# Kernel optimization log

Measured on AMD Instinct MI355X. Metric: run time of the kernel, lower is better.

Reference implementation:

```python
import jax, jax.numpy as jnp
import numpy as np

B, C, H, W = 8, 256, 64, 64
NUM_HEADS = 4


def setup_inputs() -> dict:
    key = jax.random.key(0)
    ks = jax.random.split(key, 6)
    s = 0.02  # small init scale for 1x1 conv weights
    return {
        "x": jax.random.normal(ks[0], (B, C, H, W), jnp.float32),
        "cproj": jax.random.normal(ks[1], (B, C, H, W), jnp.float32),
        "wq": jax.random.normal(ks[2], (C, C), jnp.float32) * s,
        "bq": jnp.zeros((C,), jnp.float32),
        "wkv": jax.random.normal(ks[3], (2 * C, C), jnp.float32) * s,
        "bkv": jnp.zeros((2 * C,), jnp.float32),
        "wo": jax.random.normal(ks[4], (C, C), jnp.float32) * s,  # zero_module in torch; random here for a meaningful baseline
        "bo": jnp.zeros((C,), jnp.float32),
    }


def reference(x, cproj, wq, bq, wkv, bkv, wo, bo):
    Bb, Cc, Hh, Ww = x.shape
    N = Hh * Ww
    h = NUM_HEADS
    d = Cc // h
    scale = 1.0 / jnp.sqrt(jnp.sqrt(jnp.asarray(Cc, jnp.float32)))

    xf = x.reshape(Bb, Cc, N)
    cf = cproj.reshape(Bb, Cc, N)

    # 1x1 convs == channel matmuls
    Q = jnp.einsum('oc,bcn->bon', wq, xf) + bq[None, :, None]           # (B,C,N)
    KV = jnp.einsum('oc,bcn->bon', wkv, cf) + bkv[None, :, None]        # (B,2C,N)
    K, V = KV[:, :Cc], KV[:, Cc:]

    # softmax over channel-dim-within-head for q, over spatial N for k
    q = jax.nn.softmax(Q.reshape(Bb, h, d, N) * scale, axis=2).reshape(Bb, Cc, N)
    k = jax.nn.softmax(K.reshape(Bb, h, d, N), axis=3).reshape(Bb, Cc, N)

    # linear-attention: (B,C,C) context, then project back to N — note heads are mixed, per original bmm
    context = jnp.einsum('bcn,bdn->bcd', k, V)
    out = jnp.einsum('bcd,bdn->bcn', context, q)

    out = jnp.einsum('oc,bcn->bon', wo, out) + bo[None, :, None]
    return out.reshape(Bb, Cc, Hh, Ww)
```

## Files before the change

### kernel.cpp

```cpp
#include <hip/hip_runtime.h>

#define B_ 8
#define C_ 256
#define N_ 4096
#define H_ 4
#define KVC_ 512
#define NSPLIT 8

typedef float f32x4 __attribute__((ext_vector_type(4)));
typedef __bf16 bf16x8 __attribute__((ext_vector_type(8)));
typedef unsigned short u16x8 __attribute__((ext_vector_type(8)));
typedef unsigned short u16x4 __attribute__((ext_vector_type(4)));

union BU8 { u16x8 u; bf16x8 b; };

__device__ __forceinline__ unsigned short f2bf(float f) {
  unsigned u = __float_as_uint(f);
  u += 0x7fff + ((u >> 16) & 1);
  return (unsigned short)(u >> 16);
}

__device__ __forceinline__ f32x4 mfma16(bf16x8 a, bf16x8 b, f32x4 c) {
  return __builtin_amdgcn_mfma_f32_16x16x32_bf16(a, b, c, 0, 0, 0);
}

__global__ __launch_bounds__(256) void qproj_softmax(
    const float* __restrict__ wq, const float* __restrict__ x,
    const float* __restrict__ bq, unsigned short* __restrict__ qT) {
  __shared__ unsigned short As[256][40];
  __shared__ unsigned short Bs[32][68];
  __shared__ float bql[C_];
  const int b = blockIdx.z;
  const int n0 = blockIdx.x * 64;
  const int tid = threadIdx.x;
  const int lane = tid & 63, w = tid >> 6;
  const float* xb = x + (size_t)b * C_ * N_;

  bql[tid] = bq[tid];

  f32x4 acc[16];
#pragma unroll
  for (int i = 0; i < 16; i++) acc[i] = (f32x4){0.f, 0.f, 0.f, 0.f};

  const int colL = lane & 15, kq = lane >> 4;
  for (int kc = 0; kc < C_; kc += 32) {
    __syncthreads();
#pragma unroll
    for (int i = 0; i < 8; i++) {
      int r = i * 32 + (tid >> 3), c = (tid & 7) * 4;
      float4 v = *(const float4*)&wq[r * C_ + kc + c];
      *(u16x4*)&As[r][c] = (u16x4){f2bf(v.x), f2bf(v.y), f2bf(v.z), f2bf(v.w)};
    }
#pragma unroll
    for (int i = 0; i < 2; i++) {
      int r = i * 16 + (tid >> 4), c = (tid & 15) * 4;
      float4 v = *(const float4*)&xb[(size_t)(kc + r) * N_ + n0 + c];
      *(u16x4*)&Bs[r][c] = (u16x4){f2bf(v.x), f2bf(v.y), f2bf(v.z), f2bf(v.w)};
    }
    __syncthreads();

    BU8 bu;
#pragma unroll
    for (int j = 0; j < 8; j++) bu.u[j] = Bs[kq * 8 + j][w * 16 + colL];
    bf16x8 bf = bu.b;
#pragma unroll
    for (int mt = 0; mt < 16; mt++) {
      bf16x8 af = *(const bf16x8*)&As[mt * 16 + colL][kq * 8];
      acc[mt] = mfma16(af, bf, acc[mt]);
    }
  }

  const int quad = lane >> 4;
  const int n = n0 + w * 16 + colL;
  unsigned short* qbase = qT + ((size_t)b * N_ + n) * C_;
#pragma unroll
  for (int h = 0; h < H_; h++) {
    float v[16];
    float mx = -1e30f;
#pragma unroll
    for (int i = 0; i < 4; i++) {
      int mt = 4 * h + i;
#pragma unroll
      for (int r = 0; r < 4; r++) {
        int m = mt * 16 + quad * 4 + r;
        float val = (acc[mt][r] + bql[m]) * 0.25f;
        v[i * 4 + r] = val;
        mx = fmaxf(mx, val);
      }
    }
    mx = fmaxf(mx, __shfl_xor(mx, 16));
    mx = fmaxf(mx, __shfl_xor(mx, 32));
    float s = 0.f;
#pragma unroll
    for (int j = 0; j < 16; j++) { v[j] = __expf(v[j] - mx); s += v[j]; }
    s += __shfl_xor(s, 16);
    s += __shfl_xor(s, 32);
    float inv = 1.0f / s;
#pragma unroll
    for (int i = 0; i < 4; i++) {
      u16x4 o = (u16x4){f2bf(v[i * 4 + 0] * inv), f2bf(v[i * 4 + 1] * inv),
                        f2bf(v[i * 4 + 2] * inv), f2bf(v[i * 4 + 3] * inv)};
      *(u16x4*)(qbase + (4 * h + i) * 16 + quad * 4) = o;
    }
  }
}

__global__ __launch_bounds__(256) void kvproj(
    const float* __restrict__ wkv, const float* __restrict__ cp,
    const float* __restrict__ bkv, float* __restrict__ Kf,
    unsigned short* __restrict__ Vb) {
  __shared__ unsigned short As[128][40];
  __shared__ unsigned short Bs[32][136];
  const int b = blockIdx.z;
  const int m0 = blockIdx.y * 128, n0 = blockIdx.x * 128;
  const int tid = threadIdx.x, lane = tid & 63, w = tid >> 6;
  const int m0w = (w >> 1) * 64, n0w = (w & 1) * 64;
  const int colL = lane & 15, kq = lane >> 4;
  const float* cpb = cp + (size_t)b * C_ * N_;

  f32x4 acc[4][4];
#pragma unroll
  for (int i = 0; i < 4; i++)
#pragma unroll
    for (int j = 0; j < 4; j++) acc[i][j] = (f32x4){0.f, 0.f, 0.f, 0.f};

  for (int kc = 0; kc < C_; kc += 32) {
    __syncthreads();
#pragma unroll
    for (int i = 0; i < 4; i++) {
      int r = i * 32 + (tid >> 3), c = (tid & 7) * 4;
      float4 v = *(const float4*)&wkv[(size_t)(m0 + r) * C_ + kc + c];
      *(u16x4*)&As[r][c] = (u16x4){f2bf(v.x), f2bf(v.y), f2bf(v.z), f2bf(v.w)};
    }
#pragma unroll
    for (int i = 0; i < 4; i++) {
      int r = i * 8 + (tid >> 5), c = (tid & 31) * 4;
      float4 v = *(const float4*)&cpb[(size_t)(kc + r) * N_ + n0 + c];
      *(u16x4*)&Bs[r][c] = (u16x4){f2bf(v.x), f2bf(v.y), f2bf(v.z), f2bf(v.w)};
    }
    __syncthreads();

    bf16x8 bfr[4];
#pragma unroll
    for (int nt = 0; nt < 4; nt++) {
      BU8 bu;
#pragma unroll
      for (int j = 0; j < 8; j++) bu.u[j] = Bs[kq * 8 + j][n0w + nt * 16 + colL];
      bfr[nt] = bu.b;
    }
#pragma unroll
    for (int mt = 0; mt < 4; mt++) {
      bf16x8 af = *(const bf16x8*)&As[m0w + mt * 16 + colL][kq * 8];
#pragma unroll
      for (int nt = 0; nt < 4; nt++) acc[mt][nt] = mfma16(af, bfr[nt], acc[mt][nt]);
    }
  }

  const int quad = lane >> 4;
#pragma unroll
  for (int mt = 0; mt < 4; mt++) {
#pragma unroll
    for (int r = 0; r < 4; r++) {
      int m = m0 + m0w + mt * 16 + quad * 4 + r;
      float bias = bkv[m];
#pragma unroll
      for (int nt = 0; nt < 4; nt++) {
        int n = n0 + n0w + nt * 16 + colL;
        float val = acc[mt][nt][r] + bias;
        if (m0 < C_) {
          Kf[((size_t)b * C_ + m) * N_ + n] = val;
        } else {
          Vb[((size_t)b * C_ + (m - C_)) * N_ + n] = f2bf(val);
        }
      }
    }
  }
}

__global__ __launch_bounds__(256) void ksoftmax(const float* __restrict__ Kf,
                                                unsigned short* __restrict__ kb) {
  const int b = blockIdx.x >> 8, c = blockIdx.x & 255;
  const float* row = Kf + ((size_t)b * C_ + c) * N_;
  unsigned short* orow = kb + ((size_t)b * C_ + c) * N_;
  const int t = threadIdx.x, lane = t & 63, wv = t >> 6;
  __shared__ float red[8];

  float4 v[4];
  float mx = -1e30f;
#pragma unroll
  for (int i = 0; i < 4; i++) {
    v[i] = *(const float4*)&row[i * 1024 + t * 4];
    mx = fmaxf(fmaxf(fmaxf(mx, v[i].x), fmaxf(v[i].y, v[i].z)), v[i].w);
  }
#pragma unroll
  for (int o = 32; o > 0; o >>= 1) mx = fmaxf(mx, __shfl_down(mx, o));
  if (lane == 0) red[wv] = mx;
  __syncthreads();
  mx = fmaxf(fmaxf(red[0], red[1]), fmaxf(red[2], red[3]));

  float s = 0.f;
#pragma unroll
  for (int i = 0; i < 4; i++) {
    v[i].x = __expf(v[i].x - mx); v[i].y = __expf(v[i].y - mx);
    v[i].z = __expf(v[i].z - mx); v[i].w = __expf(v[i].w - mx);
    s += v[i].x + v[i].y + v[i].z + v[i].w;
  }
#pragma unroll
  for (int o = 32; o > 0; o >>= 1) s += __shfl_down(s, o);
  if (lane == 0) red[4 + wv] = s;
  __syncthreads();
  float inv = 1.0f / (red[4] + red[5] + red[6] + red[7]);
#pragma unroll
  for (int i = 0; i < 4; i++) {
    u16x4 o = (u16x4){f2bf(v[i].x * inv), f2bf(v[i].y * inv),
                      f2bf(v[i].z * inv), f2bf(v[i].w * inv)};
    *(u16x4*)&orow[i * 1024 + t * 4] = o;
  }
}

__global__ __launch_bounds__(256) void ctx_part(
    const unsigned short* __restrict__ kb, const unsigned short* __restrict__ Vb,
    float* __restrict__ ctxp) {
  __shared__ unsigned short As[128][40];
  __shared__ unsigned short Bs[128][40];
  const int z = blockIdx.z, b = z >> 3, s = z & 7;
  const int m0 = blockIdx.y * 128, n0 = blockIdx.x * 128;
  const int tid = threadIdx.x, lane = tid & 63, w = tid >> 6;
  const int m0w = (w >> 1) * 64, n0w = (w & 1) * 64;
  const int colL = lane & 15, kq = lane >> 4;
  const unsigned short* Ab = kb + (size_t)b * C_ * N_;
  const unsigned short* Bb = Vb + (size_t)b * C_ * N_;

  f32x4 acc[4][4];
#pragma unroll
  for (int i = 0; i < 4; i++)
#pragma unroll
    for (int j = 0; j < 4; j++) acc[i][j] = (f32x4){0.f, 0.f, 0.f, 0.f};

  const int kbeg = s * (N_ / NSPLIT);
  for (int kc = kbeg; kc < kbeg + N_ / NSPLIT; kc += 32) {
    __syncthreads();
#pragma unroll
    for (int i = 0; i < 2; i++) {
      int r = i * 64 + (tid >> 2), c = (tid & 3) * 8;
      *(u16x8*)&As[r][c] = *(const u16x8*)&Ab[(size_t)(m0 + r) * N_ + kc + c];
      *(u16x8*)&Bs[r][c] = *(const u16x8*)&Bb[(size_t)(n0 + r) * N_ + kc + c];
    }
    __syncthreads();

    bf16x8 af[4], bfr[4];
#pragma unroll
    for (int mt = 0; mt < 4; mt++) af[mt] = *(const bf16x8*)&As[m0w + mt * 16 + colL][kq * 8];
#pragma unroll
    for (int nt = 0; nt < 4; nt++) bfr[nt] = *(const bf16x8*)&Bs[n0w + nt * 16 + colL][kq * 8];
#pragma unroll
    for (int mt = 0; mt < 4; mt++)
#pragma unroll
      for (int nt = 0; nt < 4; nt++) acc[mt][nt] = mfma16(af[mt], bfr[nt], acc[mt][nt]);
  }

  float* outp = ctxp + ((size_t)s * B_ + b) * C_ * C_;
  const int quad = lane >> 4;
#pragma unroll
  for (int mt = 0; mt < 4; mt++)
#pragma unroll
    for (int nt = 0; nt < 4; nt++)
#pragma unroll
      for (int r = 0; r < 4; r++) {
        int m = m0 + m0w + mt * 16 + quad * 4 + r;
        int n = n0 + n0w + nt * 16 + colL;
        outp[(size_t)m * C_ + n] = acc[mt][nt][r];
      }
}

__global__ __launch_bounds__(256) void ctx_reduce(const float* __restrict__ ctxp,
                                                  unsigned short* __restrict__ ctxs) {
  const size_t e = ((size_t)blockIdx.x * 256 + threadIdx.x) * 4;
  float4 a = {0.f, 0.f, 0.f, 0.f};
#pragma unroll
  for (int s = 0; s < NSPLIT; s++) {
    float4 v = *(const float4*)&ctxp[(size_t)s * B_ * C_ * C_ + e];
    a.x += v.x; a.y += v.y; a.z += v.z; a.w += v.w;
  }
  *(u16x4*)&ctxs[e] = (u16x4){f2bf(a.x), f2bf(a.y), f2bf(a.z), f2bf(a.w)};
}

__global__ __launch_bounds__(256) void oproj(const float* __restrict__ wo,
                                             const unsigned short* __restrict__ ctxs,
                                             unsigned short* __restrict__ ctx2) {
  __shared__ unsigned short As[128][40];
  __shared__ unsigned short Bs[32][136];
  const int b = blockIdx.z;
  const int m0 = blockIdx.y * 128, n0 = blockIdx.x * 128;
  const int tid = threadIdx.x, lane = tid & 63, w = tid >> 6;
  const int m0w = (w >> 1) * 64, n0w = (w & 1) * 64;
  const int colL = lane & 15, kq = lane >> 4;
  const unsigned short* cb = ctxs + (size_t)b * C_ * C_;

  f32x4 acc[4][4];
#pragma unroll
  for (int i = 0; i < 4; i++)
#pragma unroll
    for (int j = 0; j < 4; j++) acc[i][j] = (f32x4){0.f, 0.f, 0.f, 0.f};

  for (int kc = 0; kc < C_; kc += 32) {
    __syncthreads();
#pragma unroll
    for (int i = 0; i < 4; i++) {
      int r = i * 32 + (tid >> 3), c = (tid & 7) * 4;
      float4 v = *(const float4*)&wo[(size_t)(m0 + r) * C_ + kc + c];
      *(u16x4*)&As[r][c] = (u16x4){f2bf(v.x), f2bf(v.y), f2bf(v.z), f2bf(v.w)};
    }
#pragma unroll
    for (int i = 0; i < 2; i++) {
      int r = i * 16 + (tid >> 4), c = (tid & 15) * 8;
      *(u16x8*)&Bs[r][c] = *(const u16x8*)&cb[(size_t)(kc + r) * C_ + n0 + c];
    }
    __syncthreads();

    bf16x8 bfr[4];
#pragma unroll
    for (int nt = 0; nt < 4; nt++) {
      BU8 bu;
#pragma unroll
      for (int j = 0; j < 8; j++) bu.u[j] = Bs[kq * 8 + j][n0w + nt * 16 + colL];
      bfr[nt] = bu.b;
    }
#pragma unroll
    for (int mt = 0; mt < 4; mt++) {
      bf16x8 af = *(const bf16x8*)&As[m0w + mt * 16 + colL][kq * 8];
#pragma unroll
      for (int nt = 0; nt < 4; nt++) acc[mt][nt] = mfma16(af, bfr[nt], acc[mt][nt]);
    }
  }

  unsigned short* ob = ctx2 + (size_t)b * C_ * C_;
  const int quad = lane >> 4;
#pragma unroll
  for (int mt = 0; mt < 4; mt++)
#pragma unroll
    for (int nt = 0; nt < 4; nt++)
#pragma unroll
      for (int r = 0; r < 4; r++) {
        int m = m0 + m0w + mt * 16 + quad * 4 + r;
        int n = n0 + n0w + nt * 16 + colL;
        ob[(size_t)m * C_ + n] = f2bf(acc[mt][nt][r]);
      }
}

__global__ __launch_bounds__(256) void outgemm(const unsigned short* __restrict__ ctx2,
                                               const unsigned short* __restrict__ qT,
                                               const float* __restrict__ bo,
                                               float* __restrict__ out) {
  __shared__ unsigned short As[128][40];
  __shared__ unsigned short Bs[128][40];
  const int b = blockIdx.z;
  const int n0 = blockIdx.x * 128, m0 = blockIdx.y * 128;
  const int tid = threadIdx.x, lane = tid & 63, w = tid >> 6;
  const int m0w = (w >> 1) * 64, n0w = (w & 1) * 64;
  const int colL = lane & 15, kq = lane >> 4;
  const unsigned short* Ab = ctx2 + (size_t)b * C_ * C_;
  const unsigned short* Bb = qT + (size_t)b * N_ * C_;

  f32x4 acc[4][4];
#pragma unroll
  for (int i = 0; i < 4; i++)
#pragma unroll
    for (int j = 0; j < 4; j++) acc[i][j] = (f32x4){0.f, 0.f, 0.f, 0.f};

  for (int kc = 0; kc < C_; kc += 32) {
    __syncthreads();
#pragma unroll
    for (int i = 0; i < 2; i++) {
      int r = i * 64 + (tid >> 2), c = (tid & 3) * 8;
      *(u16x8*)&As[r][c] = *(const u16x8*)&Ab[(size_t)(m0 + r) * C_ + kc + c];
      *(u16x8*)&Bs[r][c] = *(const u16x8*)&Bb[(size_t)(n0 + r) * C_ + kc + c];
    }
    __syncthreads();

    bf16x8 af[4], bfr[4];
#pragma unroll
    for (int mt = 0; mt < 4; mt++) af[mt] = *(const bf16x8*)&As[m0w + mt * 16 + colL][kq * 8];
#pragma unroll
    for (int nt = 0; nt < 4; nt++) bfr[nt] = *(const bf16x8*)&Bs[n0w + nt * 16 + colL][kq * 8];
#pragma unroll
    for (int mt = 0; mt < 4; mt++)
#pragma unroll
      for (int nt = 0; nt < 4; nt++) acc[mt][nt] = mfma16(af[mt], bfr[nt], acc[mt][nt]);
  }

  float* ob = out + (size_t)b * C_ * N_;
  const int quad = lane >> 4;
#pragma unroll
  for (int mt = 0; mt < 4; mt++)
#pragma unroll
    for (int r = 0; r < 4; r++) {
      int m = m0 + m0w + mt * 16 + quad * 4 + r;
      float bias = bo[m];
#pragma unroll
      for (int nt = 0; nt < 4; nt++) {
        int n = n0 + n0w + nt * 16 + colL;
        ob[(size_t)m * N_ + n] = acc[mt][nt][r] + bias;
      }
    }
}

extern "C" void kernel_launch(void* const* d_in, const int* in_sizes, int n_in,
                              void* d_out, int out_size, void* d_ws, size_t ws_size,
                              hipStream_t stream) {
  const float* x     = (const float*)d_in[0];
  const float* cproj = (const float*)d_in[1];
  const float* wq    = (const float*)d_in[2];
  const float* bq    = (const float*)d_in[3];
  const float* wkv   = (const float*)d_in[4];
  const float* bkv   = (const float*)d_in[5];
  const float* wo    = (const float*)d_in[6];
  const float* bo    = (const float*)d_in[7];
  float* out = (float*)d_out;

  unsigned short* qT   = (unsigned short*)d_ws;
  float*          Kf   = (float*)(qT + (size_t)B_ * N_ * C_);
  unsigned short* Vb   = (unsigned short*)(Kf + (size_t)B_ * C_ * N_);
  unsigned short* kb   = Vb + (size_t)B_ * C_ * N_;
  float*          ctxp = (float*)(kb + (size_t)B_ * C_ * N_);
  unsigned short* ctxs = (unsigned short*)(ctxp + (size_t)NSPLIT * B_ * C_ * C_);
  unsigned short* ctx2 = ctxs + (size_t)B_ * C_ * C_;

  qproj_softmax<<<dim3(N_ / 64, 1, B_), 256, 0, stream>>>(wq, x, bq, qT);
  kvproj<<<dim3(N_ / 128, KVC_ / 128, B_), 256, 0, stream>>>(wkv, cproj, bkv, Kf, Vb);
  ksoftmax<<<dim3(B_ * C_), 256, 0, stream>>>(Kf, kb);
  ctx_part<<<dim3(2, 2, B_ * NSPLIT), 256, 0, stream>>>(kb, Vb, ctxp);
  ctx_reduce<<<dim3(B_ * C_ * C_ / 1024), 256, 0, stream>>>(ctxp, ctxs);
  oproj<<<dim3(2, 2, B_), 256, 0, stream>>>(wo, ctxs, ctx2);
  outgemm<<<dim3(N_ / 128, 2, B_), 256, 0, stream>>>(ctx2, qT, bo, out);
}
```

Measured before the change: 216.8 us.

## Pre-cast inputs to bf16 K-major and stage GEMM tiles with direct-to-LDS loads

Adds kernels that cast the weights to bf16 and transpose-cast x and cproj into N-major bf16 layouts. All GEMMs then stage 64-wide K tiles into XOR-swizzled LDS through global_load_lds, which removes the per-element LDS gathers and the in-loop float-to-bf16 conversion. The q projection is retiled to 128x128 blocks, ctx_part uses narrower tiles for more blocks, and the context reduce now writes a transposed result. Workspace buffers are aliased to save memory. The cost is two extra launches and an extra pass over the inputs for the transpose.

```diff
diff --git a/kernel.cpp b/kernel.cpp
--- a/kernel.cpp
+++ b/kernel.cpp
@@ -3,8 +3,6 @@
 #define B_ 8
 #define C_ 256
 #define N_ 4096
-#define H_ 4
-#define KVC_ 512
 #define NSPLIT 8
 
 typedef float f32x4 __attribute__((ext_vector_type(4)));
@@ -12,8 +10,6 @@
 typedef unsigned short u16x8 __attribute__((ext_vector_type(8)));
 typedef unsigned short u16x4 __attribute__((ext_vector_type(4)));
 
-union BU8 { u16x8 u; bf16x8 b; };
-
 __device__ __forceinline__ unsigned short f2bf(float f) {
   unsigned u = __float_as_uint(f);
   u += 0x7fff + ((u >> 16) & 1);
@@ -24,70 +20,118 @@
   return __builtin_amdgcn_mfma_f32_16x16x32_bf16(a, b, c, 0, 0, 0);
 }
 
-__global__ __launch_bounds__(256) void qproj_softmax(
-    const float* __restrict__ wq, const float* __restrict__ x,
+typedef __attribute__((address_space(1))) const void* gvp;
+typedef __attribute__((address_space(3))) void* lvp;
+__device__ __forceinline__ void gld16(const void* g, void* l) {
+  __builtin_amdgcn_global_load_lds((gvp)g, (lvp)l, 16, 0, 0);
+}
+
+template <int ROWS>
+__device__ __forceinline__ void stage(unsigned short* lds, const unsigned short* g,
+                                      int ld, int w, int lane) {
+  const int r8 = lane >> 3;
+  const int ce = ((lane & 7) ^ r8) << 3;
+  const unsigned short* gp = g + (size_t)(w * (ROWS / 4) + r8) * ld + ce;
+  unsigned short* lp = lds + w * (ROWS / 4) * 64;
+#pragma unroll
+  for (int i = 0; i < ROWS / 32; i++)
+    gld16(gp + (size_t)(i * 8) * ld, lp + i * 512);
+}
+
+__device__ __forceinline__ bf16x8 frag(const unsigned short* lds, int row, int kc) {
+  return *(const bf16x8*)(lds + row * 64 + ((kc ^ (row & 7)) << 3));
+}
+
+__global__ __launch_bounds__(256) void castw(
+    const float* __restrict__ wq, const float* __restrict__ wkv,
+    const float* __restrict__ wo, unsigned short* __restrict__ wqb,
+    unsigned short* __restrict__ wkvb, unsigned short* __restrict__ wob) {
+  int i = (blockIdx.x * 256 + threadIdx.x) * 4;
+  const float* src;
+  unsigned short* dst;
+  int off;
+  if (i < 65536) { src = wq; dst = wqb; off = i; }
+  else if (i < 196608) { src = wkv; dst = wkvb; off = i - 65536; }
+  else { src = wo; dst = wob; off = i - 196608; }
+  float4 v = *(const float4*)(src + off);
+  *(u16x4*)(dst + off) = (u16x4){f2bf(v.x), f2bf(v.y), f2bf(v.z), f2bf(v.w)};
+}
+
+__global__ __launch_bounds__(256) void transpose_cast(
+    const float* __restrict__ x, const float* __restrict__ cp,
+    unsigned short* __restrict__ xT, unsigned short* __restrict__ cpT) {
+  __shared__ unsigned short tr[64][72];
+  const int z = blockIdx.z, b = z >> 1;
+  const float* src = (z & 1) ? cp : x;
+  unsigned short* dst = (z & 1) ? cpT : xT;
+  const int c0 = blockIdx.y * 64, n0 = blockIdx.x * 64;
+  const int t = threadIdx.x;
+  const int row = t >> 2, cg = (t & 3) * 16;
+  const float* sp = src + ((size_t)b * C_ + c0 + row) * N_ + n0 + cg;
+#pragma unroll
+  for (int j = 0; j < 16; j += 4) {
+    float4 v = *(const float4*)(sp + j);
+    tr[cg + j + 0][row] = f2bf(v.x);
+    tr[cg + j + 1][row] = f2bf(v.y);
+    tr[cg + j + 2][row] = f2bf(v.z);
+    tr[cg + j + 3][row] = f2bf(v.w);
+  }
+  __syncthreads();
+  unsigned short* dp = dst + ((size_t)b * N_ + n0 + row) * C_ + c0 + cg;
+  *(u16x8*)dp = *(const u16x8*)&tr[row][cg];
+  *(u16x8*)(dp + 8) = *(const u16x8*)&tr[row][cg + 8];
+}
+
+__global__ __launch_bounds__(256) void qproj(
+    const unsigned short* __restrict__ wqb, const unsigned short* __restrict__ xT,
     const float* __restrict__ bq, unsigned short* __restrict__ qT) {
-  __shared__ unsigned short As[256][40];
-  __shared__ unsigned short Bs[32][68];
-  __shared__ float bql[C_];
-  const int b = blockIdx.z;
-  const int n0 = blockIdx.x * 64;
-  const int tid = threadIdx.x;
-  const int lane = tid & 63, w = tid >> 6;
-  const float* xb = x + (size_t)b * C_ * N_;
-
-  bql[tid] = bq[tid];
-
-  f32x4 acc[16];
-#pragma unroll
-  for (int i = 0; i < 16; i++) acc[i] = (f32x4){0.f, 0.f, 0.f, 0.f};
-
-  const int colL = lane & 15, kq = lane >> 4;
-  for (int kc = 0; kc < C_; kc += 32) {
-    __syncthreads();
-#pragma unroll
-    for (int i = 0; i < 8; i++) {
-      int r = i * 32 + (tid >> 3), c = (tid & 7) * 4;
-      float4 v = *(const float4*)&wq[r * C_ + kc + c];
-      *(u16x4*)&As[r][c] = (u16x4){f2bf(v.x), f2bf(v.y), f2bf(v.z), f2bf(v.w)};
-    }
-#pragma unroll
-    for (int i = 0; i < 2; i++) {
-      int r = i * 16 + (tid >> 4), c = (tid & 15) * 4;
-      float4 v = *(const float4*)&xb[(size_t)(kc + r) * N_ + n0 + c];
-      *(u16x4*)&Bs[r][c] = (u16x4){f2bf(v.x), f2bf(v.y), f2bf(v.z), f2bf(v.w)};
-    }
-    __syncthreads();
-
-    BU8 bu;
-#pragma unroll
-    for (int j = 0; j < 8; j++) bu.u[j] = Bs[kq * 8 + j][w * 16 + colL];
-    bf16x8 bf = bu.b;
-#pragma unroll
-    for (int mt = 0; mt < 16; mt++) {
-      bf16x8 af = *(const bf16x8*)&As[mt * 16 + colL][kq * 8];
-      acc[mt] = mfma16(af, bf, acc[mt]);
-    }
-  }
-
-  const int quad = lane >> 4;
-  const int n = n0 + w * 16 + colL;
-  unsigned short* qbase = qT + ((size_t)b * N_ + n) * C_;
-#pragma unroll
-  for (int h = 0; h < H_; h++) {
+  __shared__ __align__(16) unsigned short As[128 * 64];
+  __shared__ __align__(16) unsigned short Bs[128 * 64];
+  const int b = blockIdx.z, m0 = blockIdx.y * 128, n0 = blockIdx.x * 128;
+  const int tid = threadIdx.x, lane = tid & 63, w = tid >> 6;
+  const int m0w = (w >> 1) * 64, n0w = (w & 1) * 64;
+  const int colL = lane & 15, kq = lane >> 4, quad = lane >> 4;
+  const unsigned short* Ag = wqb + (size_t)m0 * C_;
+  const unsigned short* Bg = xT + ((size_t)b * N_ + n0) * C_;
+
+  f32x4 acc[4][4];
+#pragma unroll
+  for (int i = 0; i < 4; i++)
+#pragma unroll
+    for (int j = 0; j < 4; j++) acc[i][j] = (f32x4){0.f, 0.f, 0.f, 0.f};
+
+  for (int kt = 0; kt < 4; kt++) {
+    stage<128>(As, Ag + kt * 64, C_, w, lane);
+    stage<128>(Bs, Bg + kt * 64, C_, w, lane);
+    __syncthreads();
+#pragma unroll
+    for (int ks = 0; ks < 2; ks++) {
+      bf16x8 af[4], bf[4];
+#pragma unroll
+      for (int mt = 0; mt < 4; mt++) af[mt] = frag(As, m0w + mt * 16 + colL, ks * 4 + kq);
+#pragma unroll
+      for (int nt = 0; nt < 4; nt++) bf[nt] = frag(Bs, n0w + nt * 16 + colL, ks * 4 + kq);
+#pragma unroll
+      for (int mt = 0; mt < 4; mt++)
+#pragma unroll
+        for (int nt = 0; nt < 4; nt++) acc[mt][nt] = mfma16(af[mt], bf[nt], acc[mt][nt]);
+    }
+    __syncthreads();
+  }
+
+#pragma unroll
+  for (int nt = 0; nt < 4; nt++) {
     float v[16];
     float mx = -1e30f;
 #pragma unroll
-    for (int i = 0; i < 4; i++) {
-      int mt = 4 * h + i;
+    for (int mt = 0; mt < 4; mt++)
 #pragma unroll
       for (int r = 0; r < 4; r++) {
-        int m = mt * 16 + quad * 4 + r;
-        float val = (acc[mt][r] + bql[m]) * 0.25f;
-        v[i * 4 + r] = val;
+        int m = m0 + m0w + mt * 16 + quad * 4 + r;
+        float val = (acc[mt][nt][r] + bq[m]) * 0.25f;
+        v[mt * 4 + r] = val;
         mx = fmaxf(mx, val);
       }
-    }
     mx = fmaxf(mx, __shfl_xor(mx, 16));
     mx = fmaxf(mx, __shfl_xor(mx, 32));
     float s = 0.f;
@@ -96,27 +140,29 @@
     s += __shfl_xor(s, 16);
     s += __shfl_xor(s, 32);
     float inv = 1.0f / s;
-#pragma unroll
-    for (int i = 0; i < 4; i++) {
-      u16x4 o = (u16x4){f2bf(v[i * 4 + 0] * inv), f2bf(v[i * 4 + 1] * inv),
-                        f2bf(v[i * 4 + 2] * inv), f2bf(v[i * 4 + 3] * inv)};
-      *(u16x4*)(qbase + (4 * h + i) * 16 + quad * 4) = o;
+    const int n = n0 + n0w + nt * 16 + colL;
+    unsigned short* qb = qT + ((size_t)b * N_ + n) * C_ + m0 + m0w;
+#pragma unroll
+    for (int mt = 0; mt < 4; mt++) {
+      u16x4 o = (u16x4){f2bf(v[mt * 4 + 0] * inv), f2bf(v[mt * 4 + 1] * inv),
+                        f2bf(v[mt * 4 + 2] * inv), f2bf(v[mt * 4 + 3] * inv)};
+      *(u16x4*)(qb + mt * 16 + quad * 4) = o;
     }
   }
 }
 
 __global__ __launch_bounds__(256) void kvproj(
-    const float* __restrict__ wkv, const float* __restrict__ cp,
+    const unsigned short* __restrict__ wkvb, const unsigned short* __restrict__ cpT,
     const float* __restrict__ bkv, float* __restrict__ Kf,
     unsigned short* __restrict__ Vb) {
-  __shared__ unsigned short As[128][40];
-  __shared__ unsigned short Bs[32][136];
-  const int b = blockIdx.z;
-  const int m0 = blockIdx.y * 128, n0 = blockIdx.x * 128;
+  __shared__ __align__(16) unsigned short As[128 * 64];
+  __shared__ __align__(16) unsigned short Bs[128 * 64];
+  const int b = blockIdx.z, m0 = blockIdx.y * 128, n0 = blockIdx.x * 128;
   const int tid = threadIdx.x, lane = tid & 63, w = tid >> 6;
   const int m0w = (w >> 1) * 64, n0w = (w & 1) * 64;
-  const int colL = lane & 15, kq = lane >> 4;
-  const float* cpb = cp + (size_t)b * C_ * N_;
+  const int colL = lane & 15, kq = lane >> 4, quad = lane >> 4;
+  const unsigned short* Ag = wkvb + (size_t)m0 * C_;
+  const unsigned short* Bg = cpT + ((size_t)b * N_ + n0) * C_;
 
   f32x4 acc[4][4];
 #pragma unroll
@@ -124,57 +170,41 @@
 #pragma unroll
     for (int j = 0; j < 4; j++) acc[i][j] = (f32x4){0.f, 0.f, 0.f, 0.f};
 
-  for (int kc = 0; kc < C_; kc += 32) {
-    __syncthreads();
-#pragma unroll
-    for (int i = 0; i < 4; i++) {
-      int r = i * 32 + (tid >> 3), c = (tid & 7) * 4;
-      float4 v = *(const float4*)&wkv[(size_t)(m0 + r) * C_ + kc + c];
-      *(u16x4*)&As[r][c] = (u16x4){f2bf(v.x), f2bf(v.y), f2bf(v.z), f2bf(v.w)};
-    }
-#pragma unroll
-    for (int i = 0; i < 4; i++) {
-      int r = i * 8 + (tid >> 5), c = (tid & 31) * 4;
-      float4 v = *(const float4*)&cpb[(size_t)(kc + r) * N_ + n0 + c];
-      *(u16x4*)&Bs[r][c] = (u16x4){f2bf(v.x), f2bf(v.y), f2bf(v.z), f2bf(v.w)};
-    }
-    __syncthreads();
-
-    bf16x8 bfr[4];
-#pragma unroll
-    for (int nt = 0; nt < 4; nt++) {
-      BU8 bu;
-#pragma unroll
-      for (int j = 0; j < 8; j++) bu.u[j] = Bs[kq * 8 + j][n0w + nt * 16 + colL];
-      bfr[nt] = bu.b;
-    }
-#pragma unroll
-    for (int mt = 0; mt < 4; mt++) {
-      bf16x8 af = *(const bf16x8*)&As[m0w + mt * 16 + colL][kq * 8];
-#pragma unroll
-      for (int nt = 0; nt < 4; nt++) acc[mt][nt] = mfma16(af, bfr[nt], acc[mt][nt]);
-    }
-  }
-
-  const int quad = lane >> 4;
-#pragma unroll
-  for (int mt = 0; mt < 4; mt++) {
+  for (int kt = 0; kt < 4; kt++) {
+    stage<128>(As, Ag + kt * 64, C_, w, lane);
+    stage<128>(Bs, Bg + kt * 64, C_, w, lane);
+    __syncthreads();
+#pragma unroll
+    for (int ks = 0; ks < 2; ks++) {
+      bf16x8 af[4], bf[4];
+#pragma unroll
+      for (int mt = 0; mt < 4; mt++) af[mt] = frag(As, m0w + mt * 16 + colL, ks * 4 + kq);
+#pragma unroll
+      for (int nt = 0; nt < 4; nt++) bf[nt] = frag(Bs, n0w + nt * 16 + colL, ks * 4 + kq);
+#pragma unroll
+      for (int mt = 0; mt < 4; mt++)
+#pragma unroll
+        for (int nt = 0; nt < 4; nt++) acc[mt][nt] = mfma16(af[mt], bf[nt], acc[mt][nt]);
+    }
+    __syncthreads();
+  }
+
+#pragma unroll
+  for (int mt = 0; mt < 4; mt++)
 #pragma unroll
     for (int r = 0; r < 4; r++) {
       int m = m0 + m0w + mt * 16 + quad * 4 + r;
       float bias = bkv[m];
-#pragma unroll
-      for (int nt = 0; nt < 4; nt++) {
-        int n = n0 + n0w + nt * 16 + colL;
-        float val = acc[mt][nt][r] + bias;
-        if (m0 < C_) {
-          Kf[((size_t)b * C_ + m) * N_ + n] = val;
-        } else {
-          Vb[((size_t)b * C_ + (m - C_)) * N_ + n] = f2bf(val);
-        }
+      if (m < C_) {
+        float* kr = Kf + ((size_t)b * C_ + m) * N_ + n0 + n0w;
+#pragma unroll
+        for (int nt = 0; nt < 4; nt++) kr[nt * 16 + colL] = acc[mt][nt][r] + bias;
+      } else {
+        unsigned short* vr = Vb + ((size_t)b * C_ + m - C_) * N_ + n0 + n0w;
+#pragma unroll
+        for (int nt = 0; nt < 4; nt++) vr[nt * 16 + colL] = f2bf(acc[mt][nt][r] + bias);
       }
     }
-  }
 }
 
 __global__ __launch_bounds__(256) void ksoftmax(const float* __restrict__ Kf,
@@ -221,50 +251,47 @@
 __global__ __launch_bounds__(256) void ctx_part(
     const unsigned short* __restrict__ kb, const unsigned short* __restrict__ Vb,
     float* __restrict__ ctxp) {
-  __shared__ unsigned short As[128][40];
-  __shared__ unsigned short Bs[128][40];
+  __shared__ __align__(16) unsigned short As[128 * 64];
+  __shared__ __align__(16) unsigned short Bs[64 * 64];
   const int z = blockIdx.z, b = z >> 3, s = z & 7;
-  const int m0 = blockIdx.y * 128, n0 = blockIdx.x * 128;
+  const int m0 = blockIdx.y * 128, n0 = blockIdx.x * 64;
   const int tid = threadIdx.x, lane = tid & 63, w = tid >> 6;
-  const int m0w = (w >> 1) * 64, n0w = (w & 1) * 64;
-  const int colL = lane & 15, kq = lane >> 4;
-  const unsigned short* Ab = kb + (size_t)b * C_ * N_;
-  const unsigned short* Bb = Vb + (size_t)b * C_ * N_;
-
-  f32x4 acc[4][4];
+  const int m0w = (w & 1) * 64, n0w = (w >> 1) * 32;
+  const int colL = lane & 15, kq = lane >> 4, quad = lane >> 4;
+  const unsigned short* Ag = kb + ((size_t)b * C_ + m0) * N_;
+  const unsigned short* Bg = Vb + ((size_t)b * C_ + n0) * N_;
+  const int kbeg = s * (N_ / NSPLIT);
+
+  f32x4 acc[4][2];
 #pragma unroll
   for (int i = 0; i < 4; i++)
 #pragma unroll
-    for (int j = 0; j < 4; j++) acc[i][j] = (f32x4){0.f, 0.f, 0.f, 0.f};
-
-  const int kbeg = s * (N_ / NSPLIT);
-  for (int kc = kbeg; kc < kbeg + N_ / NSPLIT; kc += 32) {
-    __syncthreads();
-#pragma unroll
-    for (int i = 0; i < 2; i++) {
-      int r = i * 64 + (tid >> 2), c = (tid & 3) * 8;
-      *(u16x8*)&As[r][c] = *(const u16x8*)&Ab[(size_t)(m0 + r) * N_ + kc + c];
-      *(u16x8*)&Bs[r][c] = *(const u16x8*)&Bb[(size_t)(n0 + r) * N_ + kc + c];
-    }
-    __syncthreads();
-
-    bf16x8 af[4], bfr[4];
-#pragma unroll
-    for (int mt = 0; mt < 4; mt++) af[mt] = *(const bf16x8*)&As[m0w + mt * 16 + colL][kq * 8];
-#pragma unroll
-    for (int nt = 0; nt < 4; nt++) bfr[nt] = *(const bf16x8*)&Bs[n0w + nt * 16 + colL][kq * 8];
-#pragma unroll
-    for (int mt = 0; mt < 4; mt++)
-#pragma unroll
-      for (int nt = 0; nt < 4; nt++) acc[mt][nt] = mfma16(af[mt], bfr[nt], acc[mt][nt]);
+    for (int j = 0; j < 2; j++) acc[i][j] = (f32x4){0.f, 0.f, 0.f, 0.f};
+
+  for (int kt = 0; kt < (N_ / NSPLIT) / 64; kt++) {
+    stage<128>(As, Ag + kbeg + kt * 64, N_, w, lane);
+    stage<64>(Bs, Bg + kbeg + kt * 64, N_, w, lane);
+    __syncthreads();
+#pragma unroll
+    for (int ks = 0; ks < 2; ks++) {
+      bf16x8 af[4], bf[2];
+#pragma unroll
+      for (int mt = 0; mt < 4; mt++) af[mt] = frag(As, m0w + mt * 16 + colL, ks * 4 + kq);
+#pragma unroll
+      for (int nt = 0; nt < 2; nt++) bf[nt] = frag(Bs, n0w + nt * 16 + colL, ks * 4 + kq);
+#pragma unroll
+      for (int mt = 0; mt < 4; mt++)
+#pragma unroll
+        for (int nt = 0; nt < 2; nt++) acc[mt][nt] = mfma16(af[mt], bf[nt], acc[mt][nt]);
+    }
+    __syncthreads();
   }
 
   float* outp = ctxp + ((size_t)s * B_ + b) * C_ * C_;
-  const int quad = lane >> 4;
 #pragma unroll
   for (int mt = 0; mt < 4; mt++)
 #pragma unroll
-    for (int nt = 0; nt < 4; nt++)
+    for (int nt = 0; nt < 2; nt++)
 #pragma unroll
       for (int r = 0; r < 4; r++) {
         int m = m0 + m0w + mt * 16 + quad * 4 + r;
@@ -273,29 +300,44 @@
       }
 }
 
-__global__ __launch_bounds__(256) void ctx_reduce(const float* __restrict__ ctxp,
-                                                  unsigned short* __restrict__ ctxs) {
-  const size_t e = ((size_t)blockIdx.x * 256 + threadIdx.x) * 4;
-  float4 a = {0.f, 0.f, 0.f, 0.f};
-#pragma unroll
+__global__ __launch_bounds__(256) void ctx_reduce_t(const float* __restrict__ ctxp,
+                                                    unsigned short* __restrict__ ctxsT) {
+  __shared__ unsigned short t[64][72];
+  const int b = blockIdx.z, c0 = blockIdx.y * 64, d0 = blockIdx.x * 64;
+  const int tid = threadIdx.x;
+  const int cl = tid >> 2, dg = (tid & 3) * 16;
+  const float* base = ctxp + ((size_t)b * C_ + c0 + cl) * C_ + d0 + dg;
+  float acc[16];
+#pragma unroll
+  for (int j = 0; j < 16; j++) acc[j] = 0.f;
   for (int s = 0; s < NSPLIT; s++) {
-    float4 v = *(const float4*)&ctxp[(size_t)s * B_ * C_ * C_ + e];
-    a.x += v.x; a.y += v.y; a.z += v.z; a.w += v.w;
-  }
-  *(u16x4*)&ctxs[e] = (u16x4){f2bf(a.x), f2bf(a.y), f2bf(a.z), f2bf(a.w)};
-}
-
-__global__ __launch_bounds__(256) void oproj(const float* __restrict__ wo,
-                                             const unsigned short* __restrict__ ctxs,
-                                             unsigned short* __restrict__ ctx2) {
-  __shared__ unsigned short As[128][40];
-  __shared__ unsigned short Bs[32][136];
-  const int b = blockIdx.z;
-  const int m0 = blockIdx.y * 128, n0 = blockIdx.x * 128;
+    const float* p = base + (size_t)s * B_ * C_ * C_;
+#pragma unroll
+    for (int j = 0; j < 16; j += 4) {
+      float4 v = *(const float4*)(p + j);
+      acc[j] += v.x; acc[j + 1] += v.y; acc[j + 2] += v.z; acc[j + 3] += v.w;
+    }
+  }
+#pragma unroll
+  for (int j = 0; j < 16; j++) t[dg + j][cl] = f2bf(acc[j]);
+  __syncthreads();
+  const int dr = tid >> 2, cg = (tid & 3) * 16;
+  unsigned short* dp = ctxsT + ((size_t)b * C_ + d0 + dr) * C_ + c0 + cg;
+  *(u16x8*)dp = *(const u16x8*)&t[dr][cg];
+  *(u16x8*)(dp + 8) = *(const u16x8*)&t[dr][cg + 8];
+}
+
+__global__ __launch_bounds__(256) void oproj(
+    const unsigned short* __restrict__ wob, const unsigned short* __restrict__ ctxsT,
+    unsigned short* __restrict__ ctx2) {
+  __shared__ __align__(16) unsigned short As[128 * 64];
+  __shared__ __align__(16) unsigned short Bs[128 * 64];
+  const int b = blockIdx.z, m0 = blockIdx.y * 128, n0 = blockIdx.x * 128;
   const int tid = threadIdx.x, lane = tid & 63, w = tid >> 6;
   const int m0w = (w >> 1) * 64, n0w = (w & 1) * 64;
-  const int colL = lane & 15, kq = lane >> 4;
-  const unsigned short* cb = ctxs + (size_t)b * C_ * C_;
+  const int colL = lane & 15, kq = lane >> 4, quad = lane >> 4;
+  const unsigned short* Ag = wob + (size_t)m0 * C_;
+  const unsigned short* Bg = ctxsT + ((size_t)b * C_ + n0) * C_;
 
   f32x4 acc[4][4];
 #pragma unroll
@@ -303,39 +345,26 @@
 #pragma unroll
     for (int j = 0; j < 4; j++) acc[i][j] = (f32x4){0.f, 0.f, 0.f, 0.f};
 
-  for (int kc = 0; kc < C_; kc += 32) {
-    __syncthreads();
-#pragma unroll
-    for (int i = 0; i < 4; i++) {
-      int r = i * 32 + (tid >> 3), c = (tid & 7) * 4;
-      float4 v = *(const float4*)&wo[(size_t)(m0 + r) * C_ + kc + c];
-      *(u16x4*)&As[r][c] = (u16x4){f2bf(v.x), f2bf(v.y), f2bf(v.z), f2bf(v.w)};
-    }
-#pragma unroll
-    for (int i = 0; i < 2; i++) {
-      int r = i * 16 + (tid >> 4), c = (tid & 15) * 8;
-      *(u16x8*)&Bs[r][c] = *(const u16x8*)&cb[(size_t)(kc + r) * C_ + n0 + c];
-    }
-    __syncthreads();
-
-    bf16x8 bfr[4];
-#pragma unroll
-    for (int nt = 0; nt < 4; nt++) {
-      BU8 bu;
-#pragma unroll
-      for (int j = 0; j < 8; j++) bu.u[j] = Bs[kq * 8 + j][n0w + nt * 16 + colL];
-      bfr[nt] = bu.b;
-    }
-#pragma unroll
-    for (int mt = 0; mt < 4; mt++) {
-      bf16x8 af = *(const bf16x8*)&As[m0w + mt * 16 + colL][kq * 8];
-#pragma unroll
-      for (int nt = 0; nt < 4; nt++) acc[mt][nt] = mfma16(af, bfr[nt], acc[mt][nt]);
-    }
+  for (int kt = 0; kt < 4; kt++) {
+    stage<128>(As, Ag + kt * 64, C_, w, lane);
+    stage<128>(Bs, Bg + kt * 64, C_, w, lane);
+    __syncthreads();
+#pragma unroll
+    for (int ks = 0; ks < 2; ks++) {
+      bf16x8 af[4], bf[4];
+#pragma unroll
+      for (int mt = 0; mt < 4; mt++) af[mt] = frag(As, m0w + mt * 16 + colL, ks * 4 + kq);
+#pragma unroll
+      for (int nt = 0; nt < 4; nt++) bf[nt] = frag(Bs, n0w + nt * 16 + colL, ks * 4 + kq);
+#pragma unroll
+      for (int mt = 0; mt < 4; mt++)
+#pragma unroll
+        for (int nt = 0; nt < 4; nt++) acc[mt][nt] = mfma16(af[mt], bf[nt], acc[mt][nt]);
+    }
+    __syncthreads();
   }
 
   unsigned short* ob = ctx2 + (size_t)b * C_ * C_;
-  const int quad = lane >> 4;
 #pragma unroll
   for (int mt = 0; mt < 4; mt++)
 #pragma unroll
@@ -348,19 +377,17 @@
       }
 }
 
-__global__ __launch_bounds__(256) void outgemm(const unsigned short* __restrict__ ctx2,
-                                               const unsigned short* __restrict__ qT,
-                                               const float* __restrict__ bo,
-                                               float* __restrict__ out) {
-  __shared__ unsigned short As[128][40];
-  __shared__ unsigned short Bs[128][40];
-  const int b = blockIdx.z;
-  const int n0 = blockIdx.x * 128, m0 = blockIdx.y * 128;
+__global__ __launch_bounds__(256) void outgemm(
+    const unsigned short* __restrict__ ctx2, const unsigned short* __restrict__ qT,
+    const float* __restrict__ bo, float* __restrict__ out) {
+  __shared__ __align__(16) unsigned short As[128 * 64];
+  __shared__ __align__(16) unsigned short Bs[128 * 64];
+  const int b = blockIdx.z, n0 = blockIdx.x * 128, m0 = blockIdx.y * 128;
   const int tid = threadIdx.x, lane = tid & 63, w = tid >> 6;
   const int m0w = (w >> 1) * 64, n0w = (w & 1) * 64;
-  const int colL = lane & 15, kq = lane >> 4;
-  const unsigned short* Ab = ctx2 + (size_t)b * C_ * C_;
-  const unsigned short* Bb = qT + (size_t)b * N_ * C_;
+  const int colL = lane & 15, kq = lane >> 4, quad = lane >> 4;
+  const unsigned short* Ag = ctx2 + ((size_t)b * C_ + m0) * C_;
+  const unsigned short* Bg = qT + ((size_t)b * N_ + n0) * C_;
 
   f32x4 acc[4][4];
 #pragma unroll
@@ -368,29 +395,26 @@
 #pragma unroll
     for (int j = 0; j < 4; j++) acc[i][j] = (f32x4){0.f, 0.f, 0.f, 0.f};
 
-  for (int kc = 0; kc < C_; kc += 32) {
-    __syncthreads();
-#pragma unroll
-    for (int i = 0; i < 2; i++) {
-      int r = i * 64 + (tid >> 2), c = (tid & 3) * 8;
-      *(u16x8*)&As[r][c] = *(const u16x8*)&Ab[(size_t)(m0 + r) * C_ + kc + c];
-      *(u16x8*)&Bs[r][c] = *(const u16x8*)&Bb[(size_t)(n0 + r) * C_ + kc + c];
-    }
-    __syncthreads();
-
-    bf16x8 af[4], bfr[4];
-#pragma unroll
-    for (int mt = 0; mt < 4; mt++) af[mt] = *(const bf16x8*)&As[m0w + mt * 16 + colL][kq * 8];
-#pragma unroll
-    for (int nt = 0; nt < 4; nt++) bfr[nt] = *(const bf16x8*)&Bs[n0w + nt * 16 + colL][kq * 8];
-#pragma unroll
-    for (int mt = 0; mt < 4; mt++)
-#pragma unroll
-      for (int nt = 0; nt < 4; nt++) acc[mt][nt] = mfma16(af[mt], bfr[nt], acc[mt][nt]);
+  for (int kt = 0; kt < 4; kt++) {
+    stage<128>(As, Ag + kt * 64, C_, w, lane);
+    stage<128>(Bs, Bg + kt * 64, C_, w, lane);
+    __syncthreads();
+#pragma unroll
+    for (int ks = 0; ks < 2; ks++) {
+      bf16x8 af[4], bf[4];
+#pragma unroll
+      for (int mt = 0; mt < 4; mt++) af[mt] = frag(As, m0w + mt * 16 + colL, ks * 4 + kq);
+#pragma unroll
+      for (int nt = 0; nt < 4; nt++) bf[nt] = frag(Bs, n0w + nt * 16 + colL, ks * 4 + kq);
+#pragma unroll
+      for (int mt = 0; mt < 4; mt++)
+#pragma unroll
+        for (int nt = 0; nt < 4; nt++) acc[mt][nt] = mfma16(af[mt], bf[nt], acc[mt][nt]);
+    }
+    __syncthreads();
   }
 
   float* ob = out + (size_t)b * C_ * N_;
-  const int quad = lane >> 4;
 #pragma unroll
   for (int mt = 0; mt < 4; mt++)
 #pragma unroll
@@ -418,19 +442,26 @@
   const float* bo    = (const float*)d_in[7];
   float* out = (float*)d_out;
 
-  unsigned short* qT   = (unsigned short*)d_ws;
-  float*          Kf   = (float*)(qT + (size_t)B_ * N_ * C_);
-  unsigned short* Vb   = (unsigned short*)(Kf + (size_t)B_ * C_ * N_);
-  unsigned short* kb   = Vb + (size_t)B_ * C_ * N_;
-  float*          ctxp = (float*)(kb + (size_t)B_ * C_ * N_);
-  unsigned short* ctxs = (unsigned short*)(ctxp + (size_t)NSPLIT * B_ * C_ * C_);
-  unsigned short* ctx2 = ctxs + (size_t)B_ * C_ * C_;
-
-  qproj_softmax<<<dim3(N_ / 64, 1, B_), 256, 0, stream>>>(wq, x, bq, qT);
-  kvproj<<<dim3(N_ / 128, KVC_ / 128, B_), 256, 0, stream>>>(wkv, cproj, bkv, Kf, Vb);
-  ksoftmax<<<dim3(B_ * C_), 256, 0, stream>>>(Kf, kb);
-  ctx_part<<<dim3(2, 2, B_ * NSPLIT), 256, 0, stream>>>(kb, Vb, ctxp);
-  ctx_reduce<<<dim3(B_ * C_ * C_ / 1024), 256, 0, stream>>>(ctxp, ctxs);
-  oproj<<<dim3(2, 2, B_), 256, 0, stream>>>(wo, ctxs, ctx2);
-  outgemm<<<dim3(N_ / 128, 2, B_), 256, 0, stream>>>(ctx2, qT, bo, out);
-}
+  unsigned short* xT    = (unsigned short*)d_ws;
+  unsigned short* cpT   = xT + 8388608;
+  unsigned short* qT    = cpT + 8388608;
+  float*          Kf    = (float*)(qT + 8388608);
+  unsigned short* Vb    = (unsigned short*)(Kf + 8388608);
+  unsigned short* wqb   = Vb + 8388608;
+  unsigned short* wkvb  = wqb + 65536;
+  unsigned short* wob   = wkvb + 131072;
+  unsigned short* ctxsT = wob + 65536;
+  unsigned short* ctx2  = ctxsT + 524288;
+  unsigned short* kb    = xT;
+  float*          ctxp  = (float*)cpT;
+
+  castw<<<256, 256, 0, stream>>>(wq, wkv, wo, wqb, wkvb, wob);
+  transpose_cast<<<dim3(64, 4, 16), 256, 0, stream>>>(x, cproj, xT, cpT);
+  qproj<<<dim3(32, 2, 8), 256, 0, stream>>>(wqb, xT, bq, qT);
+  kvproj<<<dim3(32, 4, 8), 256, 0, stream>>>(wkvb, cpT, bkv, Kf, Vb);
+  ksoftmax<<<2048, 256, 0, stream>>>(Kf, kb);
+  ctx_part<<<dim3(4, 2, 64), 256, 0, stream>>>(kb, Vb, ctxp);
+  ctx_reduce_t<<<dim3(4, 4, 8), 256, 0, stream>>>(ctxp, ctxsT);
+  oproj<<<dim3(2, 2, 8), 256, 0, stream>>>(wob, ctxsT, ctx2);
+  outgemm<<<dim3(32, 2, 8), 256, 0, stream>>>(ctx2, qT, bo, out);
+}
```

New measurement: 205.2 us. 5.4% less time.
